# Kernel optimization log

Measured on AMD Instinct MI355X. Metric: run time of the kernel, lower is better.

Reference implementation:

```python
import jax, jax.numpy as jnp
import numpy as np

B, LQ, LD, H, DIM, PF = 16, 64, 2048, 1024, 128, 4
MAXK = LD // PF + 1  # static upper bound on num clusters (valid_len <= LD)


def setup_inputs() -> dict:
    key = jax.random.key(0)
    k1, k2, k3, k4 = jax.random.split(key, 4)
    return {
        "q_hidden": jax.random.normal(k1, (B, LQ, H), jnp.float32),
        "d_hidden": jax.random.normal(k2, (B, LD, H), jnp.float32),
        "W": jax.random.normal(k3, (H, DIM), jnp.float32) * (1.0 / np.sqrt(H)),  # xavier-ish
        "b": jnp.zeros((DIM,), jnp.float32),
        "q_mask": jnp.ones((B, LQ), jnp.int32),
        "d_mask": jnp.ones((B, LD), jnp.int32),
        "labels": jax.random.randint(k4, (B, LD), 0, MAXK, dtype=jnp.int32),
        "pooling_factor": PF,
    }


def _encode(hidden, W, b, mask):
    # proj -> L2 normalize -> zero out padded tokens
    r = hidden @ W + b
    r = r / jnp.clip(jnp.linalg.norm(r, axis=-1, keepdims=True), 1e-12)
    return r * mask[..., None].astype(r.dtype)


def _pool(d_repr, d_mask, labels, pf):
    # segment-mean per batch sample, cluster labels supplied externally
    Bn, L, D = d_repr.shape
    max_k = L // pf + 1  # static
    valid = jnp.clip(d_mask.sum(-1), 2, None)          # [B]
    k = valid // pf + 1                                 # per-sample num clusters
    lab = jnp.where(d_mask > 0, labels % k[:, None], max_k)  # invalid tokens -> dummy seg
    seg = lambda vals, idx: jax.ops.segment_sum(vals, idx, num_segments=max_k + 1)
    sums = jax.vmap(seg)(d_repr, lab)[:, :max_k]                          # [B,K,D]
    counts = jax.vmap(seg)(jnp.where(d_mask > 0, 1.0, 0.0), lab)[:, :max_k]
    means = sums / jnp.clip(counts, 1.0)[..., None]
    means = means / jnp.clip(jnp.linalg.norm(means, axis=-1, keepdims=True), 1e-12)
    pad_mask = jnp.arange(max_k)[None, :] < k[:, None]                    # [B,K]
    return means * pad_mask[..., None], pad_mask


def reference(q_hidden, d_hidden, W, b, q_mask, d_mask, labels, pooling_factor):
    q = _encode(q_hidden, W, b, q_mask)            # [B,LQ,DIM]
    d = _encode(d_hidden, W, b, d_mask)            # [B,LD,DIM]
    d_pool, pmask = _pool(d, d_mask, labels, pooling_factor)  # [B,K,DIM]
    sim = jnp.einsum('bqd,bkd->bqk', q, d_pool)
    sim = jnp.where(pmask[:, None, :], sim, -1e4)
    score = (sim.max(-1) * q_mask.astype(sim.dtype)).sum(-1)  # maxsum per pair
    return score
```

## Files before the change

kernel.cpp:

```cpp
#include <hip/hip_runtime.h>
#include <hip/hip_bf16.h>

#define BB    16
#define LQ    64
#define LD    2048
#define HH    1024
#define DIM   128
#define MAXK  513
#define SCH   9
#define DGRID 1024
#define QGRID 32

typedef __attribute__((ext_vector_type(8))) short short8;
typedef __attribute__((ext_vector_type(4))) float f32x4;

__device__ __forceinline__ float b2f(ushort u) {
    union { float f; unsigned int u32; } c; c.u32 = ((unsigned int)u) << 16; return c.f;
}
__device__ __forceinline__ ushort f2b_rn(float f) {
    unsigned int x = __float_as_uint(f);
    return (ushort)((x + 0x7fffu + ((x >> 16) & 1u)) >> 16);
}

__device__ __forceinline__ void gld16(void* lds, const void* g) {
    __builtin_amdgcn_global_load_lds(
        (const __attribute__((address_space(1))) unsigned int*)g,
        (__attribute__((address_space(3))) unsigned int*)lds,
        16, 0, 0);
}

__global__ __launch_bounds__(256) void prep_kb_kernel(
    const float* __restrict__ W,
    const int*   __restrict__ d_mask,
    const int*   __restrict__ pf,
    ushort*      __restrict__ Wt,
    int*         __restrict__ kvals)
{
    __shared__ int red[4];
    int bid = blockIdx.x, t = threadIdx.x;
    if (bid < 512) {
        int idx = bid * 256 + t;
        int h = idx >> 7;
        int n = idx & 127;
        Wt[n * HH + h] = f2b_rn(W[idx]);
    } else {
        int b = bid - 512;
        int lane = t & 63, wave = t >> 6;
        int s = 0;
        for (int i = t; i < LD; i += 256) s += (d_mask[b * LD + i] > 0) ? 1 : 0;
        #pragma unroll
        for (int m = 1; m < 64; m <<= 1) s += __shfl_xor(s, m);
        if (lane == 0) red[wave] = s;
        __syncthreads();
        if (t == 0) {
            int v = red[0] + red[1] + red[2] + red[3];
            if (v < 2) v = 2;
            int pfv = pf[0];
            if (pfv < 1 || pfv > LD) pfv = 4;
            kvals[b] = v / pfv + 1;
        }
    }
}

__global__ __launch_bounds__(256, 4) void encode_kernel(
    const float*  __restrict__ Xd,
    const float*  __restrict__ Xq,
    const ushort* __restrict__ Wt,
    const float*  __restrict__ bias,
    const int*    __restrict__ mask_d,
    const int*    __restrict__ mask_q,
    const int*    __restrict__ labels,
    const int*    __restrict__ kvals,
    float*        __restrict__ sums,
    float*        __restrict__ q_repr)
{
    __shared__ __align__(16) uint4 buf[2][768];
    __shared__ float ssh[32][2];

    const int bid = blockIdx.x;
    const bool isq = bid >= DGRID;
    const float* X = isq ? Xq : Xd;
    const long row0 = isq ? (long)(bid - DGRID) * 32 : (long)bid * 32;

    const int t = threadIdx.x;
    const int w = t >> 6, lane = t & 63;
    const int m16 = lane & 15, quad = lane >> 4;
    const int rh = w & 1, ch = w >> 1;

    const float*  gA  = X + (row0 + w * 8 + (lane >> 3)) * HH
                          + (((lane & 7) ^ ((lane >> 3) & 7)) * 4);
    const ushort* gB0 = Wt + (long)(w * 32 + (lane >> 2)) * HH
                           + (((lane & 3) ^ ((lane >> 4) & 3)) * 8);
    const ushort* gB1 = gB0 + 16 * HH;

    f32x4 acc[4];
    #pragma unroll
    for (int j = 0; j < 4; ++j) acc[j] = (f32x4){0.f, 0.f, 0.f, 0.f};

    gld16(&buf[0][w * 64], gA);
    gld16(&buf[0][256 + w * 128], gB0);
    gld16(&buf[0][256 + w * 128 + 64], gB1);

    const int sw = m16 & 7;
    const int bsw = m16 >> 2;
    const int au = (rh * 16 + m16) * 8;

    for (int c = 0; c < 32; ++c) {
        __syncthreads();
        const int cur = c & 1;

        if (c < 31) {
            const int nxt = cur ^ 1;
            const int ko = (c + 1) * 32;
            gld16(&buf[nxt][w * 64], gA + ko);
            gld16(&buf[nxt][256 + w * 128], gB0 + ko);
            gld16(&buf[nxt][256 + w * 128 + 64], gB1 + ko);
        }

        float4 va0 = *(const float4*)&buf[cur][au + ((2 * quad) ^ sw)];
        float4 va1 = *(const float4*)&buf[cur][au + ((2 * quad + 1) ^ sw)];
        float av[8];
        *(float4*)(av) = va0; *(float4*)(av + 4) = va1;
        short8 ah, al;
        #pragma unroll
        for (int j = 0; j < 8; ++j) {
            unsigned int ux = __float_as_uint(av[j]);
            ah[j] = (short)(ux >> 16);
            float hif = __uint_as_float(ux & 0xffff0000u);
            al[j] = (short)(__float_as_uint(av[j] - hif) >> 16);
        }

        #pragma unroll
        for (int cti = 0; cti < 4; ++cti) {
            const int ct = ch * 4 + cti;
            short8 bf = *(const short8*)&buf[cur][256 + (ct * 16 + m16) * 4 + (quad ^ bsw)];
            acc[cti] = __builtin_amdgcn_mfma_f32_16x16x32_bf16(ah, bf, acc[cti], 0, 0, 0);
            acc[cti] = __builtin_amdgcn_mfma_f32_16x16x32_bf16(al, bf, acc[cti], 0, 0, 0);
        }
    }

    float bia[4];
    #pragma unroll
    for (int cti = 0; cti < 4; ++cti) bia[cti] = bias[(ch * 4 + cti) * 16 + m16];

    float vv[4][4];
    float ssp[4] = {0.f, 0.f, 0.f, 0.f};
    #pragma unroll
    for (int cti = 0; cti < 4; ++cti)
        #pragma unroll
        for (int r = 0; r < 4; ++r) {
            vv[cti][r] = acc[cti][r] + bia[cti];
            ssp[r] += vv[cti][r] * vv[cti][r];
        }
    #pragma unroll
    for (int r = 0; r < 4; ++r) {
        ssp[r] += __shfl_xor(ssp[r], 1);
        ssp[r] += __shfl_xor(ssp[r], 2);
        ssp[r] += __shfl_xor(ssp[r], 4);
        ssp[r] += __shfl_xor(ssp[r], 8);
    }
    if (m16 == 0) {
        #pragma unroll
        for (int r = 0; r < 4; ++r) ssh[rh * 16 + quad * 4 + r][ch] = ssp[r];
    }
    __syncthreads();

    #pragma unroll
    for (int r = 0; r < 4; ++r) {
        int rowl = rh * 16 + quad * 4 + r;
        long rowg = row0 + rowl;
        float ss = ssh[rowl][0] + ssh[rowl][1];
        float scale = 1.0f / fmaxf(sqrtf(ss), 1e-12f);
        if (isq) {
            scale *= (float)mask_q[rowg];
            #pragma unroll
            for (int cti = 0; cti < 4; ++cti)
                q_repr[rowg * DIM + (ch * 4 + cti) * 16 + m16] = vv[cti][r] * scale;
        } else if (mask_d[rowg] > 0) {
            int b = (int)(rowg >> 11);
            int seg = labels[rowg] % kvals[b];
            float* sp = sums + ((long)b * MAXK + seg) * DIM + m16;
            #pragma unroll
            for (int cti = 0; cti < 4; ++cti)
                atomicAdd(sp + (ch * 4 + cti) * 16, vv[cti][r] * scale);
        }
    }
}

__global__ __launch_bounds__(256) void simmax_kernel(
    const float* __restrict__ q_repr,
    const float* __restrict__ sums,
    const int*   __restrict__ kvals,
    float*       __restrict__ pmax)
{
    __shared__ __align__(16) ushort Qh[64 * 136];
    __shared__ __align__(16) ushort Ql[64 * 136];
    __shared__ __align__(16) ushort Ch[64 * 136];
    __shared__ float cn[64];

    int b = blockIdx.x / SCH, chunk = blockIdx.x % SCH;
    int t = threadIdx.x, w = t >> 6, lane = t & 63;
    int m16 = lane & 15, quad = lane >> 4;

    #pragma unroll
    for (int i = 0; i < 8; ++i) {
        int flat = i * 256 + t;
        int row = flat >> 5, c4 = flat & 31;
        float4 v = *(const float4*)(q_repr + ((long)b * LQ + row) * DIM + c4 * 4);
        float x[4]; *(float4*)x = v;
        ushort4 h, l;
        ushort* hp = (ushort*)&h; ushort* lp = (ushort*)&l;
        #pragma unroll
        for (int j = 0; j < 4; ++j) {
            unsigned int ux = __float_as_uint(x[j]);
            hp[j] = (ushort)(ux >> 16);
            lp[j] = f2b_rn(x[j] - __uint_as_float(ux & 0xffff0000u));
        }
        *(ushort4*)&Qh[row * 136 + c4 * 4] = h;
        *(ushort4*)&Ql[row * 136 + c4 * 4] = l;
    }
    #pragma unroll
    for (int i = 0; i < 8; ++i) {
        int flat = i * 256 + t;
        int row = flat >> 5, c4 = flat & 31;
        int kk = chunk * 64 + row;
        float4 v = (kk < MAXK)
            ? *(const float4*)(sums + ((long)b * MAXK + kk) * DIM + c4 * 4)
            : make_float4(0.f, 0.f, 0.f, 0.f);
        ushort4 h; ushort* hp = (ushort*)&h;
        hp[0] = f2b_rn(v.x); hp[1] = f2b_rn(v.y);
        hp[2] = f2b_rn(v.z); hp[3] = f2b_rn(v.w);
        *(ushort4*)&Ch[row * 136 + c4 * 4] = h;
    }
    __syncthreads();

    {
        int c = w * 16 + m16;
        float ssv = 0.f;
        #pragma unroll
        for (int j = 0; j < 16; ++j) {
            unsigned int u = *(const unsigned int*)&Ch[c * 136 + quad * 32 + j * 2];
            float x0 = b2f((ushort)u), x1 = b2f((ushort)(u >> 16));
            ssv += x0 * x0 + x1 * x1;
        }
        ssv += __shfl_xor(ssv, 16);
        ssv += __shfl_xor(ssv, 32);
        if (quad == 0) cn[c] = (ssv > 1e-24f) ? rsqrtf(ssv) : 0.f;
    }
    __syncthreads();

    f32x4 acc[4];
    #pragma unroll
    for (int j = 0; j < 4; ++j) acc[j] = (f32x4){0.f, 0.f, 0.f, 0.f};

    #pragma unroll
    for (int kc = 0; kc < 4; ++kc) {
        short8 qh = *(const short8*)&Qh[(w * 16 + m16) * 136 + kc * 32 + quad * 8];
        short8 ql = *(const short8*)&Ql[(w * 16 + m16) * 136 + kc * 32 + quad * 8];
        #pragma unroll
        for (int ct = 0; ct < 4; ++ct) {
            short8 cf = *(const short8*)&Ch[(ct * 16 + m16) * 136 + kc * 32 + quad * 8];
            acc[ct] = __builtin_amdgcn_mfma_f32_16x16x32_bf16(qh, cf, acc[ct], 0, 0, 0);
            acc[ct] = __builtin_amdgcn_mfma_f32_16x16x32_bf16(ql, cf, acc[ct], 0, 0, 0);
        }
    }

    int kb = kvals[b];
    #pragma unroll
    for (int r = 0; r < 4; ++r) {
        float mx = -1e4f;
        #pragma unroll
        for (int ct = 0; ct < 4; ++ct) {
            int cl = chunk * 64 + ct * 16 + m16;
            float sim = acc[ct][r] * cn[ct * 16 + m16];
            mx = fmaxf(mx, (cl < kb) ? sim : -1e4f);
        }
        mx = fmaxf(mx, __shfl_xor(mx, 1));
        mx = fmaxf(mx, __shfl_xor(mx, 2));
        mx = fmaxf(mx, __shfl_xor(mx, 4));
        mx = fmaxf(mx, __shfl_xor(mx, 8));
        if (m16 == 0)
            pmax[((long)b * SCH + chunk) * 64 + w * 16 + quad * 4 + r] = mx;
    }
}

__global__ __launch_bounds__(64) void final_kernel(
    const float* __restrict__ pmax,
    const int*   __restrict__ q_mask,
    float*       __restrict__ out)
{
    int b = blockIdx.x, r = threadIdx.x;
    float m = -3e38f;
    #pragma unroll
    for (int c = 0; c < SCH; ++c)
        m = fmaxf(m, pmax[((long)b * SCH + c) * 64 + r]);
    m *= (float)q_mask[b * LQ + r];
    #pragma unroll
    for (int sh = 1; sh < 64; sh <<= 1) m += __shfl_xor(m, sh);
    if (r == 0) out[b] = m;
}

extern "C" void kernel_launch(void* const* d_in, const int* in_sizes, int n_in,
                              void* d_out, int out_size, void* d_ws, size_t ws_size,
                              hipStream_t stream) {
    const float* q_hidden = (const float*)d_in[0];
    const float* d_hidden = (const float*)d_in[1];
    const float* W        = (const float*)d_in[2];
    const float* bias     = (const float*)d_in[3];
    const int*   q_mask   = (const int*)d_in[4];
    const int*   d_mask   = (const int*)d_in[5];
    const int*   labels   = (const int*)d_in[6];
    const int*   pf       = (const int*)d_in[7];

    float* ws     = (float*)d_ws;
    float* q_repr = ws;
    float* sums   = q_repr + (long)BB * LQ * DIM;
    float* pmaxb  = sums + (long)BB * MAXK * DIM;
    int*   kvals  = (int*)(pmaxb + BB * SCH * 64);
    ushort* Wt    = (ushort*)(kvals + 16);

    hipMemsetAsync(sums, 0, (size_t)BB * MAXK * DIM * sizeof(float), stream);

    prep_kb_kernel<<<512 + BB, 256, 0, stream>>>(W, d_mask, pf, Wt, kvals);
    encode_kernel<<<DGRID + QGRID, 256, 0, stream>>>(d_hidden, q_hidden, Wt, bias,
                                                     d_mask, q_mask, labels, kvals,
                                                     sums, q_repr);
    simmax_kernel<<<BB * SCH, 256, 0, stream>>>(q_repr, sums, kvals, pmaxb);
    final_kernel<<<BB, 64, 0, stream>>>(pmaxb, q_mask, (float*)d_out);
}
```

Before: 259.2 us.

## Replace global atomic pooling with separate LDS-accumulating segment-sum kernel

The encode epilogue now writes normalized document representations to a workspace buffer instead of scattering global atomicAdds into cluster sums. A new pool kernel, one block per batch and 16-column slice, accumulates segment sums in shared memory and writes them out, which also removes the memset. This trades global atomic contention for an extra round trip of the document representation through memory and an additional launch with limited parallelism.

```diff
diff --git a/kernel.cpp b/kernel.cpp
--- a/kernel.cpp
+++ b/kernel.cpp
@@ -69,9 +69,7 @@
     const float*  __restrict__ bias,
     const int*    __restrict__ mask_d,
     const int*    __restrict__ mask_q,
-    const int*    __restrict__ labels,
-    const int*    __restrict__ kvals,
-    float*        __restrict__ sums,
+    float*        __restrict__ d_repr,
     float*        __restrict__ q_repr)
 {
     __shared__ __align__(16) uint4 buf[2][768];
@@ -176,14 +174,51 @@
             #pragma unroll
             for (int cti = 0; cti < 4; ++cti)
                 q_repr[rowg * DIM + (ch * 4 + cti) * 16 + m16] = vv[cti][r] * scale;
-        } else if (mask_d[rowg] > 0) {
-            int b = (int)(rowg >> 11);
-            int seg = labels[rowg] % kvals[b];
-            float* sp = sums + ((long)b * MAXK + seg) * DIM + m16;
+        } else {
+            scale *= (float)mask_d[rowg];
             #pragma unroll
             for (int cti = 0; cti < 4; ++cti)
-                atomicAdd(sp + (ch * 4 + cti) * 16, vv[cti][r] * scale);
-        }
+                d_repr[rowg * DIM + (ch * 4 + cti) * 16 + m16] = vv[cti][r] * scale;
+        }
+    }
+}
+
+__global__ __launch_bounds__(256) void pool_kernel(
+    const float* __restrict__ d_repr,
+    const int*   __restrict__ labels,
+    const int*   __restrict__ kvals,
+    float*       __restrict__ sums)
+{
+    __shared__ float acc[MAXK][17];
+
+    const int b  = blockIdx.x >> 3;
+    const int dc = (blockIdx.x & 7) * 16;
+    const int t  = threadIdx.x;
+
+    for (int i = t; i < MAXK * 17; i += 256) (&acc[0][0])[i] = 0.f;
+    __syncthreads();
+
+    const int kb = kvals[b];
+    #pragma unroll
+    for (int i = 0; i < LD / 256; ++i) {
+        const int row = i * 256 + t;
+        const long g = (long)b * LD + row;
+        const int seg = labels[g] % kb;
+        const float* p = d_repr + g * DIM + dc;
+        #pragma unroll
+        for (int j = 0; j < 4; ++j) {
+            float4 v = *(const float4*)(p + j * 4);
+            atomicAdd(&acc[seg][j * 4 + 0], v.x);
+            atomicAdd(&acc[seg][j * 4 + 1], v.y);
+            atomicAdd(&acc[seg][j * 4 + 2], v.z);
+            atomicAdd(&acc[seg][j * 4 + 3], v.w);
+        }
+    }
+    __syncthreads();
+
+    for (int i = t; i < MAXK * 16; i += 256) {
+        const int seg = i >> 4, j = i & 15;
+        sums[((long)b * MAXK + seg) * DIM + dc + j] = acc[seg][j];
     }
 }
 
@@ -318,13 +353,12 @@
     float* pmaxb  = sums + (long)BB * MAXK * DIM;
     int*   kvals  = (int*)(pmaxb + BB * SCH * 64);
     ushort* Wt    = (ushort*)(kvals + 16);
-
-    hipMemsetAsync(sums, 0, (size_t)BB * MAXK * DIM * sizeof(float), stream);
+    float* d_repr = (float*)(Wt + (long)HH * DIM);
 
     prep_kb_kernel<<<512 + BB, 256, 0, stream>>>(W, d_mask, pf, Wt, kvals);
     encode_kernel<<<DGRID + QGRID, 256, 0, stream>>>(d_hidden, q_hidden, Wt, bias,
-                                                     d_mask, q_mask, labels, kvals,
-                                                     sums, q_repr);
+                                                     d_mask, q_mask, d_repr, q_repr);
+    pool_kernel<<<BB * 8, 256, 0, stream>>>(d_repr, labels, kvals, sums);
     simmax_kernel<<<BB * SCH, 256, 0, stream>>>(q_repr, sums, kvals, pmaxb);
     final_kernel<<<BB, 64, 0, stream>>>(pmaxb, q_mask, (float*)d_out);
 }
```

Measured after the change: 297.1 us. 14.6% more time.

## Deepen encode GEMM pipeline to 4 stages, tile W transpose, fuse memset

Applied to the files above, without the earlier changes.

The encode kernel's global-to-LDS prefetch goes from double-buffered to a 4-buffer ring with 3 chunks in flight. It uses explicit vmcnt waits and raw barriers in place of __syncthreads, and launch bounds drop to 3 waves/SIMD to fit the larger LDS. The W transpose to bf16 now goes through a shared-memory tile so the Wt stores are coalesced. The sums hipMemsetAsync is folded into the prep kernel as extra zeroing blocks, which removes one launch/memset op. The deeper pipeline costs occupancy, and the hand-written waitcnt counts must match the number of loads issued.

```diff
diff --git a/kernel.cpp b/kernel.cpp
--- a/kernel.cpp
+++ b/kernel.cpp
@@ -34,17 +34,30 @@
     const int*   __restrict__ d_mask,
     const int*   __restrict__ pf,
     ushort*      __restrict__ Wt,
-    int*         __restrict__ kvals)
+    int*         __restrict__ kvals,
+    float*       __restrict__ sums)
 {
-    __shared__ int red[4];
     int bid = blockIdx.x, t = threadIdx.x;
-    if (bid < 512) {
-        int idx = bid * 256 + t;
-        int h = idx >> 7;
-        int n = idx & 127;
-        Wt[n * HH + h] = f2b_rn(W[idx]);
-    } else {
-        int b = bid - 512;
+    if (bid < 16) {
+        __shared__ ushort tile[128][72];
+        const int h0 = bid * 64;
+        #pragma unroll
+        for (int i = 0; i < 32; ++i) {
+            int flat = i * 256 + t;
+            int r = flat >> 7, c = flat & 127;
+            tile[c][r] = f2b_rn(W[(long)(h0 + r) * DIM + c]);
+        }
+        __syncthreads();
+        #pragma unroll
+        for (int i = 0; i < 4; ++i) {
+            int flat = i * 256 + t;
+            int n = flat >> 3, u = flat & 7;
+            uint4 v = *(const uint4*)&tile[n][u * 8];
+            *(uint4*)&Wt[(long)n * HH + h0 + u * 8] = v;
+        }
+    } else if (bid < 32) {
+        __shared__ int red[4];
+        int b = bid - 16;
         int lane = t & 63, wave = t >> 6;
         int s = 0;
         for (int i = t; i < LD; i += 256) s += (d_mask[b * LD + i] > 0) ? 1 : 0;
@@ -59,10 +72,16 @@
             if (pfv < 1 || pfv > LD) pfv = 4;
             kvals[b] = v / pfv + 1;
         }
-    }
-}
-
-__global__ __launch_bounds__(256, 4) void encode_kernel(
+    } else {
+        const int total4 = (BB * MAXK * DIM) / 4;
+        float4* s4 = (float4*)sums;
+        const float4 z = make_float4(0.f, 0.f, 0.f, 0.f);
+        for (int i = (bid - 32) * 256 + t; i < total4; i += 256 * 256)
+            s4[i] = z;
+    }
+}
+
+__global__ __launch_bounds__(256, 3) void encode_kernel(
     const float*  __restrict__ Xd,
     const float*  __restrict__ Xq,
     const ushort* __restrict__ Wt,
@@ -74,7 +93,7 @@
     float*        __restrict__ sums,
     float*        __restrict__ q_repr)
 {
-    __shared__ __align__(16) uint4 buf[2][768];
+    __shared__ __align__(16) uint4 buf[4][768];
     __shared__ float ssh[32][2];
 
     const int bid = blockIdx.x;
@@ -97,26 +116,19 @@
     #pragma unroll
     for (int j = 0; j < 4; ++j) acc[j] = (f32x4){0.f, 0.f, 0.f, 0.f};
 
-    gld16(&buf[0][w * 64], gA);
-    gld16(&buf[0][256 + w * 128], gB0);
-    gld16(&buf[0][256 + w * 128 + 64], gB1);
+    #pragma unroll
+    for (int p = 0; p < 3; ++p) {
+        const int ko = p * 32;
+        gld16(&buf[p][w * 64], gA + ko);
+        gld16(&buf[p][256 + w * 128], gB0 + ko);
+        gld16(&buf[p][256 + w * 128 + 64], gB1 + ko);
+    }
 
     const int sw = m16 & 7;
     const int bsw = m16 >> 2;
     const int au = (rh * 16 + m16) * 8;
 
-    for (int c = 0; c < 32; ++c) {
-        __syncthreads();
-        const int cur = c & 1;
-
-        if (c < 31) {
-            const int nxt = cur ^ 1;
-            const int ko = (c + 1) * 32;
-            gld16(&buf[nxt][w * 64], gA + ko);
-            gld16(&buf[nxt][256 + w * 128], gB0 + ko);
-            gld16(&buf[nxt][256 + w * 128 + 64], gB1 + ko);
-        }
-
+    auto compute = [&](int cur) {
         float4 va0 = *(const float4*)&buf[cur][au + ((2 * quad) ^ sw)];
         float4 va1 = *(const float4*)&buf[cur][au + ((2 * quad + 1) ^ sw)];
         float av[8];
@@ -129,7 +141,6 @@
             float hif = __uint_as_float(ux & 0xffff0000u);
             al[j] = (short)(__float_as_uint(av[j] - hif) >> 16);
         }
-
         #pragma unroll
         for (int cti = 0; cti < 4; ++cti) {
             const int ct = ch * 4 + cti;
@@ -137,7 +148,31 @@
             acc[cti] = __builtin_amdgcn_mfma_f32_16x16x32_bf16(ah, bf, acc[cti], 0, 0, 0);
             acc[cti] = __builtin_amdgcn_mfma_f32_16x16x32_bf16(al, bf, acc[cti], 0, 0, 0);
         }
-    }
+    };
+
+    for (int c = 0; c < 29; ++c) {
+        asm volatile("s_waitcnt vmcnt(6)" ::: "memory");
+        __builtin_amdgcn_s_barrier();
+        __builtin_amdgcn_sched_barrier(0);
+        const int nxt = (c + 3) & 3;
+        const int ko = (c + 3) * 32;
+        gld16(&buf[nxt][w * 64], gA + ko);
+        gld16(&buf[nxt][256 + w * 128], gB0 + ko);
+        gld16(&buf[nxt][256 + w * 128 + 64], gB1 + ko);
+        compute(c & 3);
+    }
+    asm volatile("s_waitcnt vmcnt(6)" ::: "memory");
+    __builtin_amdgcn_s_barrier();
+    __builtin_amdgcn_sched_barrier(0);
+    compute(1);
+    asm volatile("s_waitcnt vmcnt(3)" ::: "memory");
+    __builtin_amdgcn_s_barrier();
+    __builtin_amdgcn_sched_barrier(0);
+    compute(2);
+    asm volatile("s_waitcnt vmcnt(0)" ::: "memory");
+    __builtin_amdgcn_s_barrier();
+    __builtin_amdgcn_sched_barrier(0);
+    compute(3);
 
     float bia[4];
     #pragma unroll
@@ -319,9 +354,7 @@
     int*   kvals  = (int*)(pmaxb + BB * SCH * 64);
     ushort* Wt    = (ushort*)(kvals + 16);
 
-    hipMemsetAsync(sums, 0, (size_t)BB * MAXK * DIM * sizeof(float), stream);
-
-    prep_kb_kernel<<<512 + BB, 256, 0, stream>>>(W, d_mask, pf, Wt, kvals);
+    prep_kb_kernel<<<288, 256, 0, stream>>>(W, d_mask, pf, Wt, kvals, sums);
     encode_kernel<<<DGRID + QGRID, 256, 0, stream>>>(d_hidden, q_hidden, Wt, bias,
                                                      d_mask, q_mask, labels, kvals,
                                                      sums, q_repr);
```

Measured after the change: 265.9 us. +2.6%, slower.
